# Performance work log

Measured on AMD Instinct MI355X. Metric: run time of the kernel, lower is better.

## Reference

```python
import jax, jax.numpy as jnp
import numpy as np
from jax import lax

STRIDE = (1, 1)
PADDING = (1, 1)


def setup_inputs() -> dict:
    key = jax.random.key(0)
    k1, k2 = jax.random.split(key)
    x = jax.random.normal(k1, (32, 128, 56, 56), dtype=jnp.float32)
    kernels = jax.random.normal(k2, (256, 128, 3, 3), dtype=jnp.float32)
    return {"x": x, "kernels": kernels}


def reference(x, kernels):
    # Equivalent to the python-loop correlation conv: NCHW input, OIHW weight,
    # cross-correlation (no kernel flip), stride/padding per module config.
    out = lax.conv_general_dilated(
        x, kernels,
        window_strides=STRIDE,
        padding=[(PADDING[0], PADDING[0]), (PADDING[1], PADDING[1])],
        dimension_numbers=("NCHW", "OIHW", "NCHW"),
    )
    return out
```

## Files before the change

kernel.cpp:

```cpp
#include <hip/hip_runtime.h>
#include <cstdint>

#define N_IMG 32
#define C_IN 128
#define H_IN 56
#define W_IN 56
#define K_OUT 256
#define HW (H_IN * W_IN)
#define M_TOTAL (N_IMG * HW)
#define XP_H 58
#define XP_W 58
#define XP_ELEMS (N_IMG * XP_H * XP_W * C_IN)
#define WT_ELEMS (9 * K_OUT * C_IN)
#define N_STAGE 36

typedef __bf16 bf16x8 __attribute__((ext_vector_type(8)));
typedef float f32x4 __attribute__((ext_vector_type(4)));

__device__ __align__(16) unsigned short g_xp[XP_ELEMS];
__device__ __align__(16) unsigned short g_wt[WT_ELEMS];

static __device__ __forceinline__ unsigned short f2bf(float f) {
    unsigned int u = __builtin_bit_cast(unsigned int, f);
    u += 0x7fffu + ((u >> 16) & 1u);
    return (unsigned short)(u >> 16);
}

static __device__ __forceinline__ void async_copy16(const unsigned short* g, unsigned short* l) {
    auto gp = (const __attribute__((address_space(1))) unsigned int*)g;
    auto lp = (__attribute__((address_space(3))) unsigned int*)l;
    __builtin_amdgcn_global_load_lds(gp, lp, 16, 0, 0);
}

__global__ __launch_bounds__(256) void xpose_x(const float* __restrict__ x) {
    __shared__ float tile[C_IN * 57];
    const int h = blockIdx.x;
    const int n = blockIdx.y;
    const int tid = threadIdx.x;

    if (tid < 32) {
        int col = (tid >> 4) * (XP_W - 1);
        int q = tid & 15;
        uint4* dst = (uint4*)(g_xp + ((size_t)(n * XP_H + h + 1) * XP_W + col) * C_IN) + q;
        *dst = uint4{0u, 0u, 0u, 0u};
    }
    if (h == 0 || h == H_IN - 1) {
        int hp = (h == 0) ? 0 : XP_H - 1;
        uint4* base = (uint4*)(g_xp + ((size_t)(n * XP_H + hp) * XP_W) * C_IN);
        for (int q = tid; q < (XP_W * C_IN) / 8; q += 256) base[q] = uint4{0u, 0u, 0u, 0u};
    }

#pragma unroll
    for (int i = 0; i < 28; i++) {
        int e = i * 256 + tid;
        int c = e / 56;
        int w = e - c * 56;
        tile[c * 57 + w] = x[((n * C_IN + c) * H_IN + h) * W_IN + w];
    }
    __syncthreads();
    unsigned int* outp = (unsigned int*)g_xp;
#pragma unroll
    for (int i = 0; i < 14; i++) {
        int u = i * 256 + tid;
        int w = u >> 6;
        int cp = u & 63;
        float a = tile[(2 * cp) * 57 + w];
        float b = tile[(2 * cp + 1) * 57 + w];
        unsigned int pk = (unsigned int)f2bf(a) | ((unsigned int)f2bf(b) << 16);
        int idx = ((n * XP_H + h + 1) * XP_W + (w + 1)) * C_IN + 2 * cp;
        outp[idx >> 1] = pk;
    }
}

__global__ __launch_bounds__(256) void xpose_w(const float* __restrict__ w) {
    int e = blockIdx.x * 256 + threadIdx.x;
    int rr = e >> 15;
    int rem = e & 32767;
    int k = rem >> 7;
    int c = rem & 127;
    g_wt[e] = f2bf(w[(k * C_IN + c) * 9 + rr]);
}

__global__ __launch_bounds__(256, 4) void conv_main(float* __restrict__ out) {
    __shared__ __align__(16) unsigned short As[2][128 * 32];
    __shared__ __align__(16) unsigned short Bs[2][128 * 32];
    const unsigned short* xp = g_xp;
    const unsigned short* wt = g_wt;

    const int tid = threadIdx.x;
    const int m0 = blockIdx.x * 128;
    const int k0 = blockIdx.y * 128;
    const int wave = tid >> 6, lane = tid & 63;
    const int wm = (wave & 1) * 64;
    const int wn = (wave >> 1) * 64;
    const int lr = lane & 15;
    const int lq = lane >> 4;

    int a_base[2], b_base[2], lds_off[2];
#pragma unroll
    for (int j = 0; j < 2; j++) {
        int u = j * 256 + tid;
        int ml = u >> 2;
        int cg = u & 3;
        int p = m0 + ml;
        int n = p / HW;
        int rem = p - n * HW;
        int h = rem / W_IN;
        int w = rem - h * W_IN;
        a_base[j] = ((n * XP_H + h) * XP_W + w) * C_IN + cg * 8;
        b_base[j] = (k0 + ml) * C_IN + cg * 8;
        lds_off[j] = (j * 256 + wave * 64) * 8;
    }

    auto issue = [&](int s, int buf) {
        int rs = s >> 2;
        int c0 = (s & 3) << 5;
        int r = (rs * 11) >> 5;
        int sc = rs - r * 3;
        int a_off = (r * XP_W + sc) * C_IN + c0;
        int b_off = rs * (K_OUT * C_IN) + c0;
#pragma unroll
        for (int j = 0; j < 2; j++) {
            async_copy16(xp + a_base[j] + a_off, &As[buf][0] + lds_off[j]);
            async_copy16(wt + b_base[j] + b_off, &Bs[buf][0] + lds_off[j]);
        }
    };

    f32x4 acc[4][4];
#pragma unroll
    for (int mi = 0; mi < 4; mi++)
#pragma unroll
        for (int ni = 0; ni < 4; ni++)
            acc[mi][ni] = f32x4{0.f, 0.f, 0.f, 0.f};

    issue(0, 0);
#pragma unroll 2
    for (int s = 0; s < N_STAGE; s++) {
        const int cb = s & 1;
        __syncthreads();
        if (s + 1 < N_STAGE) issue(s + 1, cb ^ 1);
        bf16x8 af[4], bfr[4];
#pragma unroll
        for (int i = 0; i < 4; i++)
            af[i] = *(const bf16x8*)(&As[cb][0] + (wm + i * 16 + lr) * 32 + lq * 8);
#pragma unroll
        for (int i = 0; i < 4; i++)
            bfr[i] = *(const bf16x8*)(&Bs[cb][0] + (wn + i * 16 + lr) * 32 + lq * 8);
#pragma unroll
        for (int mi = 0; mi < 4; mi++)
#pragma unroll
            for (int ni = 0; ni < 4; ni++)
                acc[mi][ni] = __builtin_amdgcn_mfma_f32_16x16x32_bf16(
                    af[mi], bfr[ni], acc[mi][ni], 0, 0, 0);
    }

#pragma unroll
    for (int mi = 0; mi < 4; mi++) {
        int p = m0 + wm + mi * 16 + lq * 4;
        int n = p / HW;
        int off = p - n * HW;
#pragma unroll
        for (int ni = 0; ni < 4; ni++) {
            int k = k0 + wn + ni * 16 + lr;
            *(f32x4*)(out + (n * K_OUT + k) * HW + off) = acc[mi][ni];
        }
    }
}

extern "C" void kernel_launch(void* const* d_in, const int* in_sizes, int n_in,
                              void* d_out, int out_size, void* d_ws, size_t ws_size,
                              hipStream_t stream) {
    const float* x = (const float*)d_in[0];
    const float* w = (const float*)d_in[1];
    float* out = (float*)d_out;

    hipLaunchKernelGGL(xpose_x, dim3(H_IN, N_IMG), dim3(256), 0, stream, x);
    hipLaunchKernelGGL(xpose_w, dim3(WT_ELEMS / 256), dim3(256), 0, stream, w);
    hipLaunchKernelGGL(conv_main, dim3(M_TOTAL / 128, K_OUT / 128), dim3(256), 0, stream, out);
}
```

Baseline: 254.8 us.

## Enlarge conv GEMM tile to 256x256 with swizzled LDS and interleaved MFMA schedule

Rewrites the implicit-GEMM conv main kernel to use 512-thread blocks computing a 256x256 output tile over all output channels, with a K step of 64 per stage instead of 32. LDS tiles use an XOR swizzle to avoid bank conflicts. The loop interleaves fragment loads, barriers, priority hints and four MFMA sub-phases with the next tile's async global-to-LDS copies. Block indices are remapped to group M tiles for locality. The aim is more operand reuse per byte loaded and better load/compute overlap, at the cost of heavier register pressure (128 accumulator floats per thread) and fewer resident blocks.

```diff
diff --git a/kernel.cpp b/kernel.cpp
--- a/kernel.cpp
+++ b/kernel.cpp
@@ -12,7 +12,7 @@
 #define XP_W 58
 #define XP_ELEMS (N_IMG * XP_H * XP_W * C_IN)
 #define WT_ELEMS (9 * K_OUT * C_IN)
-#define N_STAGE 36
+#define NKT 18
 
 typedef __bf16 bf16x8 __attribute__((ext_vector_type(8)));
 typedef float f32x4 __attribute__((ext_vector_type(4)));
@@ -81,87 +81,207 @@
     g_wt[e] = f2bf(w[(k * C_IN + c) * 9 + rr]);
 }
 
-__global__ __launch_bounds__(256, 4) void conv_main(float* __restrict__ out) {
-    __shared__ __align__(16) unsigned short As[2][128 * 32];
-    __shared__ __align__(16) unsigned short Bs[2][128 * 32];
-    const unsigned short* xp = g_xp;
-    const unsigned short* wt = g_wt;
+__global__ __launch_bounds__(512, 2) void conv_main(float* __restrict__ out) {
+    __shared__ __align__(16) unsigned short As[2][16384];
+    __shared__ __align__(16) unsigned short Bs[2][16384];
+    const unsigned short* __restrict__ xp = g_xp;
+    const unsigned short* __restrict__ wt = g_wt;
 
     const int tid = threadIdx.x;
-    const int m0 = blockIdx.x * 128;
-    const int k0 = blockIdx.y * 128;
     const int wave = tid >> 6, lane = tid & 63;
-    const int wm = (wave & 1) * 64;
-    const int wn = (wave >> 1) * 64;
-    const int lr = lane & 15;
-    const int lq = lane >> 4;
-
-    int a_base[2], b_base[2], lds_off[2];
+    const int lr = lane & 15, lq = lane >> 4;
+    const int wr = wave >> 2;
+    const int wc = wave & 3;
+
+    const int bid = blockIdx.x;
+    const int m0 = ((bid & 7) * 49 + (bid >> 3)) * 256;
+
+    int a_src[2][2], b_src[2][2], lds_u[2];
 #pragma unroll
     for (int j = 0; j < 2; j++) {
-        int u = j * 256 + tid;
-        int ml = u >> 2;
-        int cg = u & 3;
-        int p = m0 + ml;
-        int n = p / HW;
-        int rem = p - n * HW;
-        int h = rem / W_IN;
-        int w = rem - h * W_IN;
-        a_base[j] = ((n * XP_H + h) * XP_W + w) * C_IN + cg * 8;
-        b_base[j] = (k0 + ml) * C_IN + cg * 8;
-        lds_off[j] = (j * 256 + wave * 64) * 8;
-    }
-
-    auto issue = [&](int s, int buf) {
-        int rs = s >> 2;
-        int c0 = (s & 3) << 5;
-        int r = (rs * 11) >> 5;
-        int sc = rs - r * 3;
-        int a_off = (r * XP_W + sc) * C_IN + c0;
-        int b_off = rs * (K_OUT * C_IN) + c0;
-#pragma unroll
-        for (int j = 0; j < 2; j++) {
-            async_copy16(xp + a_base[j] + a_off, &As[buf][0] + lds_off[j]);
-            async_copy16(wt + b_base[j] + b_off, &Bs[buf][0] + lds_off[j]);
+        const int u = j * 512 + tid;
+        const int rowl = u >> 3;
+        const int sw = ((u & 7) ^ (rowl & 7)) * 8;
+        lds_u[j] = (j * 512 + wave * 64) * 8;
+#pragma unroll
+        for (int hh = 0; hh < 2; hh++) {
+            int p = m0 + hh * 128 + rowl;
+            int n = p / HW;
+            int rem = p - n * HW;
+            int h = rem / W_IN;
+            int w = rem - h * W_IN;
+            a_src[j][hh] = ((n * XP_H + h) * XP_W + w) * C_IN + sw;
+            b_src[j][hh] = (hh * 128 + rowl) * C_IN + sw;
         }
+    }
+
+    int csw[2];
+#pragma unroll
+    for (int ks = 0; ks < 2; ks++)
+        csw[ks] = (ks * 32 + lq * 8) ^ ((lr & 7) << 3);
+    const int arow = (wr * 128 + lr) * 64;
+    const int brow = (wc * 64 + lr) * 64;
+
+    auto stage_tile = [&](int kt, int nb) {
+        const int rs = kt >> 1;
+        const int r = (rs * 11) >> 5;
+        const int sc = rs - r * 3;
+        const int aoff = (r * XP_W + sc) * C_IN + (kt & 1) * 64;
+        const int boff = rs * (K_OUT * C_IN) + (kt & 1) * 64;
+#pragma unroll
+        for (int hh = 0; hh < 2; hh++)
+#pragma unroll
+            for (int j = 0; j < 2; j++) {
+                async_copy16(xp + a_src[j][hh] + aoff, &As[nb][hh * 8192 + lds_u[j]]);
+                async_copy16(wt + b_src[j][hh] + boff, &Bs[nb][hh * 8192 + lds_u[j]]);
+            }
     };
 
-    f32x4 acc[4][4];
-#pragma unroll
-    for (int mi = 0; mi < 4; mi++)
+    f32x4 acc[8][4];
+#pragma unroll
+    for (int mi = 0; mi < 8; mi++)
+#pragma unroll
+        for (int ni = 0; ni < 4; ni++) acc[mi][ni] = f32x4{0.f, 0.f, 0.f, 0.f};
+
+    stage_tile(0, 0);
+    stage_tile(1, 1);
+    asm volatile("s_waitcnt vmcnt(8)" ::: "memory");
+    __builtin_amdgcn_s_barrier();
+    asm volatile("" ::: "memory");
+
+    for (int t = 0; t < NKT - 1; ++t) {
+        const int b = t & 1;
+        bf16x8 a0[4][2], bL[2][2], bH[2][2], a1[4][2];
+
+#pragma unroll
+        for (int mi = 0; mi < 4; mi++)
+#pragma unroll
+            for (int ks = 0; ks < 2; ks++)
+                a0[mi][ks] = *(const bf16x8*)(&As[b][arow + mi * 1024 + csw[ks]]);
+#pragma unroll
+        for (int ni = 0; ni < 2; ni++)
+#pragma unroll
+            for (int ks = 0; ks < 2; ks++)
+                bL[ni][ks] = *(const bf16x8*)(&Bs[b][brow + ni * 1024 + csw[ks]]);
+        __builtin_amdgcn_s_barrier();
+        asm volatile("s_waitcnt lgkmcnt(0)" ::: "memory");
+        __builtin_amdgcn_s_setprio(1);
+#pragma unroll
+        for (int ks = 0; ks < 2; ks++)
+#pragma unroll
+            for (int mi = 0; mi < 4; mi++)
+#pragma unroll
+                for (int ni = 0; ni < 2; ni++)
+                    acc[mi][ni] = __builtin_amdgcn_mfma_f32_16x16x32_bf16(
+                        a0[mi][ks], bL[ni][ks], acc[mi][ni], 0, 0, 0);
+        __builtin_amdgcn_s_setprio(0);
+        __builtin_amdgcn_s_barrier();
+        asm volatile("" ::: "memory");
+
+#pragma unroll
+        for (int ni = 0; ni < 2; ni++)
+#pragma unroll
+            for (int ks = 0; ks < 2; ks++)
+                bH[ni][ks] = *(const bf16x8*)(&Bs[b][brow + (ni + 2) * 1024 + csw[ks]]);
+        __builtin_amdgcn_s_barrier();
+        asm volatile("s_waitcnt lgkmcnt(0)" ::: "memory");
+        __builtin_amdgcn_s_setprio(1);
+#pragma unroll
+        for (int ks = 0; ks < 2; ks++)
+#pragma unroll
+            for (int mi = 0; mi < 4; mi++)
+#pragma unroll
+                for (int ni = 0; ni < 2; ni++)
+                    acc[mi][ni + 2] = __builtin_amdgcn_mfma_f32_16x16x32_bf16(
+                        a0[mi][ks], bH[ni][ks], acc[mi][ni + 2], 0, 0, 0);
+        __builtin_amdgcn_s_setprio(0);
+        __builtin_amdgcn_s_barrier();
+        asm volatile("" ::: "memory");
+
+#pragma unroll
+        for (int mi = 0; mi < 4; mi++)
+#pragma unroll
+            for (int ks = 0; ks < 2; ks++)
+                a1[mi][ks] = *(const bf16x8*)(&As[b][arow + (mi + 4) * 1024 + csw[ks]]);
+        __builtin_amdgcn_s_barrier();
+        asm volatile("s_waitcnt lgkmcnt(0)" ::: "memory");
+        __builtin_amdgcn_s_setprio(1);
+#pragma unroll
+        for (int ks = 0; ks < 2; ks++)
+#pragma unroll
+            for (int mi = 0; mi < 4; mi++)
+#pragma unroll
+                for (int ni = 0; ni < 2; ni++)
+                    acc[mi + 4][ni + 2] = __builtin_amdgcn_mfma_f32_16x16x32_bf16(
+                        a1[mi][ks], bH[ni][ks], acc[mi + 4][ni + 2], 0, 0, 0);
+        __builtin_amdgcn_s_setprio(0);
+        __builtin_amdgcn_s_barrier();
+        asm volatile("" ::: "memory");
+
+        if (t + 2 < NKT) stage_tile(t + 2, b);
+        __builtin_amdgcn_s_setprio(1);
+#pragma unroll
+        for (int ks = 0; ks < 2; ks++)
+#pragma unroll
+            for (int mi = 0; mi < 4; mi++)
+#pragma unroll
+                for (int ni = 0; ni < 2; ni++)
+                    acc[mi + 4][ni] = __builtin_amdgcn_mfma_f32_16x16x32_bf16(
+                        a1[mi][ks], bL[ni][ks], acc[mi + 4][ni], 0, 0, 0);
+        __builtin_amdgcn_s_setprio(0);
+        if (t + 2 < NKT) {
+            asm volatile("s_waitcnt vmcnt(8)" ::: "memory");
+        } else {
+            asm volatile("s_waitcnt vmcnt(0)" ::: "memory");
+        }
+        __builtin_amdgcn_s_barrier();
+        asm volatile("" ::: "memory");
+    }
+
+    {
+        constexpr int b = 1;
+        bf16x8 af[4][2], bb[4][2];
 #pragma unroll
         for (int ni = 0; ni < 4; ni++)
-            acc[mi][ni] = f32x4{0.f, 0.f, 0.f, 0.f};
-
-    issue(0, 0);
-#pragma unroll 2
-    for (int s = 0; s < N_STAGE; s++) {
-        const int cb = s & 1;
-        __syncthreads();
-        if (s + 1 < N_STAGE) issue(s + 1, cb ^ 1);
-        bf16x8 af[4], bfr[4];
-#pragma unroll
-        for (int i = 0; i < 4; i++)
-            af[i] = *(const bf16x8*)(&As[cb][0] + (wm + i * 16 + lr) * 32 + lq * 8);
-#pragma unroll
-        for (int i = 0; i < 4; i++)
-            bfr[i] = *(const bf16x8*)(&Bs[cb][0] + (wn + i * 16 + lr) * 32 + lq * 8);
+#pragma unroll
+            for (int ks = 0; ks < 2; ks++)
+                bb[ni][ks] = *(const bf16x8*)(&Bs[b][brow + ni * 1024 + csw[ks]]);
 #pragma unroll
         for (int mi = 0; mi < 4; mi++)
 #pragma unroll
-            for (int ni = 0; ni < 4; ni++)
-                acc[mi][ni] = __builtin_amdgcn_mfma_f32_16x16x32_bf16(
-                    af[mi], bfr[ni], acc[mi][ni], 0, 0, 0);
-    }
-
-#pragma unroll
-    for (int mi = 0; mi < 4; mi++) {
-        int p = m0 + wm + mi * 16 + lq * 4;
+            for (int ks = 0; ks < 2; ks++)
+                af[mi][ks] = *(const bf16x8*)(&As[b][arow + mi * 1024 + csw[ks]]);
+#pragma unroll
+        for (int ks = 0; ks < 2; ks++)
+#pragma unroll
+            for (int mi = 0; mi < 4; mi++)
+#pragma unroll
+                for (int ni = 0; ni < 4; ni++)
+                    acc[mi][ni] = __builtin_amdgcn_mfma_f32_16x16x32_bf16(
+                        af[mi][ks], bb[ni][ks], acc[mi][ni], 0, 0, 0);
+#pragma unroll
+        for (int mi = 0; mi < 4; mi++)
+#pragma unroll
+            for (int ks = 0; ks < 2; ks++)
+                af[mi][ks] = *(const bf16x8*)(&As[b][arow + (mi + 4) * 1024 + csw[ks]]);
+#pragma unroll
+        for (int ks = 0; ks < 2; ks++)
+#pragma unroll
+            for (int mi = 0; mi < 4; mi++)
+#pragma unroll
+                for (int ni = 0; ni < 4; ni++)
+                    acc[mi + 4][ni] = __builtin_amdgcn_mfma_f32_16x16x32_bf16(
+                        af[mi][ks], bb[ni][ks], acc[mi + 4][ni], 0, 0, 0);
+    }
+
+#pragma unroll
+    for (int mi = 0; mi < 8; mi++) {
+        int p = m0 + wr * 128 + mi * 16 + lq * 4;
         int n = p / HW;
         int off = p - n * HW;
 #pragma unroll
         for (int ni = 0; ni < 4; ni++) {
-            int k = k0 + wn + ni * 16 + lr;
+            int k = wc * 64 + ni * 16 + lr;
             *(f32x4*)(out + (n * K_OUT + k) * HW + off) = acc[mi][ni];
         }
     }
@@ -176,5 +296,5 @@
 
     hipLaunchKernelGGL(xpose_x, dim3(H_IN, N_IMG), dim3(256), 0, stream, x);
     hipLaunchKernelGGL(xpose_w, dim3(WT_ELEMS / 256), dim3(256), 0, stream, w);
-    hipLaunchKernelGGL(conv_main, dim3(M_TOTAL / 128, K_OUT / 128), dim3(256), 0, stream, out);
-}
+    hipLaunchKernelGGL(conv_main, dim3(M_TOTAL / 256), dim3(512), 0, stream, out);
+}
```

Result: faster. 229.9 us (-9.8%).

## Enlarge conv tile to 256x128 with 512 threads, swizzled LDS, split-phase pipeline

Applied to the files above, without the earlier changes.

Raises the block tile to 256 output pixels by 128 output channels with 8 waves, so weight tiles are reused across more pixels. LDS rows are XOR-swizzled to avoid bank conflicts on the fragment reads, and blocks are remapped so neighbouring blocks share data in L2. The main loop is restructured with raw barriers, explicit waitcnt, setprio and a prefetch issued between two halves of the MFMA work, so global loads overlap compute. The hand-written vmcnt counts and barrier ordering depend on exact instruction counts and can cause races if they are off. Register pressure at 512 threads with 4 blocks per CU is also a risk.

```diff
diff --git a/kernel.cpp b/kernel.cpp
--- a/kernel.cpp
+++ b/kernel.cpp
@@ -12,7 +12,7 @@
 #define XP_W 58
 #define XP_ELEMS (N_IMG * XP_H * XP_W * C_IN)
 #define WT_ELEMS (9 * K_OUT * C_IN)
-#define N_STAGE 36
+#define NKT 36
 
 typedef __bf16 bf16x8 __attribute__((ext_vector_type(8)));
 typedef float f32x4 __attribute__((ext_vector_type(4)));
@@ -81,87 +81,118 @@
     g_wt[e] = f2bf(w[(k * C_IN + c) * 9 + rr]);
 }
 
-__global__ __launch_bounds__(256, 4) void conv_main(float* __restrict__ out) {
-    __shared__ __align__(16) unsigned short As[2][128 * 32];
-    __shared__ __align__(16) unsigned short Bs[2][128 * 32];
-    const unsigned short* xp = g_xp;
-    const unsigned short* wt = g_wt;
+__global__ __launch_bounds__(512, 4) void conv_main(float* __restrict__ out) {
+    __shared__ __align__(16) unsigned short As[2][8192];
+    __shared__ __align__(16) unsigned short Bs[2][4096];
+    const unsigned short* __restrict__ xp = g_xp;
+    const unsigned short* __restrict__ wt = g_wt;
 
     const int tid = threadIdx.x;
-    const int m0 = blockIdx.x * 128;
-    const int k0 = blockIdx.y * 128;
     const int wave = tid >> 6, lane = tid & 63;
-    const int wm = (wave & 1) * 64;
-    const int wn = (wave >> 1) * 64;
-    const int lr = lane & 15;
-    const int lq = lane >> 4;
-
-    int a_base[2], b_base[2], lds_off[2];
+    const int lr = lane & 15, lq = lane >> 4;
+    const int wmL = (wave >> 1) * 64;
+    const int wnL = (wave & 1) * 64;
+
+    const int bid = blockIdx.x;
+    const int g = (bid & 7) * 98 + (bid >> 3);
+    const int m0 = (g >> 1) * 256;
+    const int k0 = (g & 1) * 128;
+
+    int a_src[2], lds_a[2];
 #pragma unroll
     for (int j = 0; j < 2; j++) {
-        int u = j * 256 + tid;
-        int ml = u >> 2;
-        int cg = u & 3;
-        int p = m0 + ml;
+        const int u = j * 512 + tid;
+        const int row = u >> 2, seg = u & 3;
+        const int sw = (seg ^ (row & 3)) * 8;
+        int p = m0 + row;
         int n = p / HW;
         int rem = p - n * HW;
         int h = rem / W_IN;
         int w = rem - h * W_IN;
-        a_base[j] = ((n * XP_H + h) * XP_W + w) * C_IN + cg * 8;
-        b_base[j] = (k0 + ml) * C_IN + cg * 8;
-        lds_off[j] = (j * 256 + wave * 64) * 8;
-    }
-
-    auto issue = [&](int s, int buf) {
-        int rs = s >> 2;
-        int c0 = (s & 3) << 5;
-        int r = (rs * 11) >> 5;
-        int sc = rs - r * 3;
-        int a_off = (r * XP_W + sc) * C_IN + c0;
-        int b_off = rs * (K_OUT * C_IN) + c0;
-#pragma unroll
-        for (int j = 0; j < 2; j++) {
-            async_copy16(xp + a_base[j] + a_off, &As[buf][0] + lds_off[j]);
-            async_copy16(wt + b_base[j] + b_off, &Bs[buf][0] + lds_off[j]);
+        a_src[j] = ((n * XP_H + h) * XP_W + w) * C_IN + sw;
+        lds_a[j] = (j * 512 + wave * 64) * 8;
+    }
+    const int brow_s = tid >> 2, bseg = tid & 3;
+    const int b_src = (k0 + brow_s) * C_IN + (bseg ^ (brow_s & 3)) * 8;
+    const int lds_b = wave * 64 * 8;
+
+    const int csw = (lq ^ (lr & 3)) * 8;
+
+    auto stage_tile = [&](int kt, int nb) {
+        const int rs = kt >> 2;
+        const int r = (rs * 11) >> 5;
+        const int sc = rs - r * 3;
+        const int aoff = (r * XP_W + sc) * C_IN + (kt & 3) * 32;
+        const int boff = rs * (K_OUT * C_IN) + (kt & 3) * 32;
+#pragma unroll
+        for (int j = 0; j < 2; j++)
+            async_copy16(xp + a_src[j] + aoff, &As[nb][lds_a[j]]);
+        async_copy16(wt + b_src + boff, &Bs[nb][lds_b]);
+    };
+
+    f32x4 acc[4][4];
+#pragma unroll
+    for (int mi = 0; mi < 4; mi++)
+#pragma unroll
+        for (int ni = 0; ni < 4; ni++) acc[mi][ni] = f32x4{0.f, 0.f, 0.f, 0.f};
+
+    stage_tile(0, 0);
+    stage_tile(1, 1);
+    asm volatile("s_waitcnt vmcnt(3)" ::: "memory");
+    __builtin_amdgcn_s_barrier();
+    asm volatile("" ::: "memory");
+
+#pragma unroll 2
+    for (int t = 0; t < NKT; ++t) {
+        const int b = t & 1;
+        bf16x8 af[4], bfv[4];
+
+#pragma unroll
+        for (int mi = 0; mi < 4; mi++)
+            af[mi] = *(const bf16x8*)(&As[b][(wmL + mi * 16 + lr) * 32 + csw]);
+#pragma unroll
+        for (int ni = 0; ni < 4; ni++)
+            bfv[ni] = *(const bf16x8*)(&Bs[b][(wnL + ni * 16 + lr) * 32 + csw]);
+        __builtin_amdgcn_s_barrier();
+        asm volatile("s_waitcnt lgkmcnt(0)" ::: "memory");
+        __builtin_amdgcn_sched_barrier(0);
+        __builtin_amdgcn_s_setprio(1);
+#pragma unroll
+        for (int mi = 0; mi < 4; mi++)
+#pragma unroll
+            for (int ni = 0; ni < 2; ni++)
+                acc[mi][ni] = __builtin_amdgcn_mfma_f32_16x16x32_bf16(
+                    af[mi], bfv[ni], acc[mi][ni], 0, 0, 0);
+        __builtin_amdgcn_s_setprio(0);
+        __builtin_amdgcn_s_barrier();
+        asm volatile("" ::: "memory");
+
+        if (t + 2 < NKT) stage_tile(t + 2, b);
+        __builtin_amdgcn_s_setprio(1);
+#pragma unroll
+        for (int mi = 0; mi < 4; mi++)
+#pragma unroll
+            for (int ni = 2; ni < 4; ni++)
+                acc[mi][ni] = __builtin_amdgcn_mfma_f32_16x16x32_bf16(
+                    af[mi], bfv[ni], acc[mi][ni], 0, 0, 0);
+        __builtin_amdgcn_s_setprio(0);
+        if (t + 2 < NKT) {
+            asm volatile("s_waitcnt vmcnt(3)" ::: "memory");
+        } else {
+            asm volatile("s_waitcnt vmcnt(0)" ::: "memory");
         }
-    };
-
-    f32x4 acc[4][4];
-#pragma unroll
-    for (int mi = 0; mi < 4; mi++)
-#pragma unroll
-        for (int ni = 0; ni < 4; ni++)
-            acc[mi][ni] = f32x4{0.f, 0.f, 0.f, 0.f};
-
-    issue(0, 0);
-#pragma unroll 2
-    for (int s = 0; s < N_STAGE; s++) {
-        const int cb = s & 1;
-        __syncthreads();
-        if (s + 1 < N_STAGE) issue(s + 1, cb ^ 1);
-        bf16x8 af[4], bfr[4];
-#pragma unroll
-        for (int i = 0; i < 4; i++)
-            af[i] = *(const bf16x8*)(&As[cb][0] + (wm + i * 16 + lr) * 32 + lq * 8);
-#pragma unroll
-        for (int i = 0; i < 4; i++)
-            bfr[i] = *(const bf16x8*)(&Bs[cb][0] + (wn + i * 16 + lr) * 32 + lq * 8);
-#pragma unroll
-        for (int mi = 0; mi < 4; mi++)
-#pragma unroll
-            for (int ni = 0; ni < 4; ni++)
-                acc[mi][ni] = __builtin_amdgcn_mfma_f32_16x16x32_bf16(
-                    af[mi], bfr[ni], acc[mi][ni], 0, 0, 0);
+        __builtin_amdgcn_s_barrier();
+        asm volatile("" ::: "memory");
     }
 
 #pragma unroll
     for (int mi = 0; mi < 4; mi++) {
-        int p = m0 + wm + mi * 16 + lq * 4;
+        int p = m0 + wmL + mi * 16 + lq * 4;
         int n = p / HW;
         int off = p - n * HW;
 #pragma unroll
         for (int ni = 0; ni < 4; ni++) {
-            int k = k0 + wn + ni * 16 + lr;
+            int k = k0 + wnL + ni * 16 + lr;
             *(f32x4*)(out + (n * K_OUT + k) * HW + off) = acc[mi][ni];
         }
     }
@@ -176,5 +207,5 @@
 
     hipLaunchKernelGGL(xpose_x, dim3(H_IN, N_IMG), dim3(256), 0, stream, x);
     hipLaunchKernelGGL(xpose_w, dim3(WT_ELEMS / 256), dim3(256), 0, stream, w);
-    hipLaunchKernelGGL(conv_main, dim3(M_TOTAL / 128, K_OUT / 128), dim3(256), 0, stream, out);
-}
+    hipLaunchKernelGGL(conv_main, dim3((M_TOTAL / 256) * (K_OUT / 128)), dim3(512), 0, stream, out);
+}
```

Result: faster. 230.8 us (-9.4%).
